# Performance work log

Hardware: AMD Instinct MI355X
Metric: run time of the kernel (lower is better)

## Reference

```python
import jax, jax.numpy as jnp
import numpy as np

EPS = 0.1
MAX_ITER = 10
N, IN_SIZE, IN_DIM = 16, 1024, 1024
HEADS, OUT_SIZE, OUT_DIM = 4, 128, 1024


def xavier(key, shape):
    fan_in, fan_out = shape[-1], int(np.prod(shape[:-1]))
    lim = float(np.sqrt(6.0 / (fan_in + fan_out)))
    return jax.random.uniform(key, shape, jnp.float32, -lim, lim)


def setup_inputs() -> dict:
    key = jax.random.key(0)
    k1, k2, k3 = jax.random.split(key, 3)
    x = jax.random.normal(k1, (N, IN_SIZE, IN_DIM), jnp.float32)
    ot_weight = xavier(k2, (HEADS, OUT_SIZE, IN_DIM))
    lin_w = xavier(k3, (OUT_DIM, HEADS * IN_DIM))
    lin_b = jnp.zeros((OUT_DIM,), jnp.float32)
    return {"x": x, "ot_weight": ot_weight, "lin_w": lin_w, "lin_b": lin_b}


def log_sinkhorn(K, max_iter):
    # K: [B, in_size, out_size] (already divided by eps)
    B, in_size, out_size = K.shape
    a = jnp.log(jnp.asarray(out_size / in_size, K.dtype))
    u = jnp.zeros((B, in_size), K.dtype)
    v = jnp.zeros((B, out_size), K.dtype)

    def body(carry, _):
        u, v = carry
        u = a - jax.nn.logsumexp(K + u[:, :, None] + v[:, None, :], axis=-1)
        v = -jax.nn.logsumexp(K + u[:, :, None] + v[:, None, :], axis=-2)
        return (u, v), None

    (u, v), _ = jax.lax.scan(body, (u, v), None, length=max_iter)
    return jnp.exp(K + u[:, :, None] + v[:, None, :])  # transport plan T


def reference(x, ot_weight, lin_w, lin_b):
    n, in_size, in_dim = x.shape
    m, out_size, _ = ot_weight.shape
    # similarity / eps : [n, m, in_size, out_size]
    K = jnp.einsum('nid,msd->nmis', x, ot_weight) / EPS
    T = log_sinkhorn(K.reshape(n * m, in_size, out_size), MAX_ITER)
    T = T.reshape(n, m, in_size, out_size)
    # weighted aggregation: [n, out_size, m, in_dim] -> [n, out_size, m*in_dim]
    feat = jnp.einsum('nmis,nid->nsmd', T, x).reshape(n, out_size, m * in_dim)
    # Linear + ReLU (Dropout is identity in eval mode)
    out = jax.nn.relu(feat @ lin_w.T + lin_b)
    return out
```

## Files before the change

### kernel.cpp

```cpp
#include <hip/hip_runtime.h>
#include <math.h>

#define EPSV 0.1f
#define MAX_ITER 10
constexpr int NB       = 16;
constexpr int IN_SIZE  = 1024;
constexpr int IN_DIM   = 1024;
constexpr int HEADS    = 4;
constexpr int OUT_SIZE = 128;
constexpr int OUT_DIM  = 1024;

typedef __attribute__((ext_vector_type(8))) _Float16 f16x8;
typedef __attribute__((ext_vector_type(4))) float f32x4;

__device__ __forceinline__ unsigned cvth2(float lo, float hi) {
    _Float16 a = (_Float16)lo, b = (_Float16)hi;
    unsigned short ua = *(unsigned short*)&a, ub = *(unsigned short*)&b;
    return (unsigned)ua | ((unsigned)ub << 16);
}
__device__ __forceinline__ unsigned short cvth1(float f) {
    _Float16 a = (_Float16)f;
    return *(unsigned short*)&a;
}
__device__ __forceinline__ unsigned short bf16rne(float f) {
    unsigned a = __float_as_uint(f);
    return (unsigned short)((a + 0x7fffu + ((a >> 16) & 1u)) >> 16);
}

template<int AMODE, bool B_F32, int CMODE, int NF, bool AKBLK, bool SWAP>
__global__ __launch_bounds__(256)
void mfma_gemm(const void* __restrict__ Ap, const void* __restrict__ Bp,
               const float* __restrict__ bias, void* __restrict__ Cp,
               int K, int lda, int ldb, int ldc, int div,
               long AsN, long AsM, long BsN, long BsM, long CsN, long CsM,
               long AkStride, float alpha)
{
    constexpr int BN  = NF * 32;
    constexpr int BKP = 40;
    const int z  = SWAP ? blockIdx.x : blockIdx.z;
    const int n0 = (SWAP ? blockIdx.z : blockIdx.x) * BN;
    const long aoff = (long)(z / div) * AsN + (long)(z % div) * AsM;
    const long boff = (long)(z / div) * BsN + (long)(z % div) * BsM;
    const long coff = (long)(z / div) * CsN + (long)(z % div) * CsM;

    __shared__ short As[128 * BKP];
    __shared__ short Bs[BN * BKP];

    const int t = threadIdx.x;
    const int lane = t & 63;
    const int w = t >> 6, wr = w >> 1, wc = w & 1;

    f32x4 acc[4][NF];
    #pragma unroll
    for (int i = 0; i < 4; ++i)
        #pragma unroll
        for (int j = 0; j < NF; ++j) { acc[i][j].x = 0.f; acc[i][j].y = 0.f; acc[i][j].z = 0.f; acc[i][j].w = 0.f; }

    for (int k0 = 0; k0 < K; k0 += 32) {
        const long abase = AKBLK ? aoff + (long)(k0 >> 10) * AkStride + (k0 & 1023)
                                 : aoff + k0;
        const long bbase = boff + k0;
        #pragma unroll
        for (int itr = 0; itr < 2; ++itr) {
            const int idx = itr * 256 + t;
            const int row = idx >> 2, kq = idx & 3;
            const uint4 p = *(const uint4*)((const short*)Ap + abase + (long)row * lda + kq * 8);
            *(uint4*)&As[row * BKP + kq * 8] = p;
        }
        #pragma unroll
        for (int itr = 0; itr < BN / 64; ++itr) {
            const int idx = itr * 256 + t;
            const int row = idx >> 2, kq = idx & 3;
            uint4 p;
            if (B_F32) {
                const float* s = (const float*)Bp + bbase + (long)(n0 + row) * ldb + kq * 8;
                const float4 f0 = *(const float4*)s, f1 = *(const float4*)(s + 4);
                p.x = cvth2(f0.x, f0.y); p.y = cvth2(f0.z, f0.w);
                p.z = cvth2(f1.x, f1.y); p.w = cvth2(f1.z, f1.w);
            } else {
                p = *(const uint4*)((const short*)Bp + bbase + (long)(n0 + row) * ldb + kq * 8);
            }
            *(uint4*)&Bs[row * BKP + kq * 8] = p;
        }
        __syncthreads();

        f16x8 af[4], bfr[NF];
        #pragma unroll
        for (int mi = 0; mi < 4; ++mi)
            af[mi] = *(const f16x8*)&As[(wr * 64 + mi * 16 + (lane & 15)) * BKP + (lane >> 4) * 8];
        #pragma unroll
        for (int ni = 0; ni < NF; ++ni)
            bfr[ni] = *(const f16x8*)&Bs[(wc * (BN / 2) + ni * 16 + (lane & 15)) * BKP + (lane >> 4) * 8];
        #pragma unroll
        for (int mi = 0; mi < 4; ++mi)
            #pragma unroll
            for (int ni = 0; ni < NF; ++ni)
                acc[mi][ni] = __builtin_amdgcn_mfma_f32_16x16x32_f16(af[mi], bfr[ni], acc[mi][ni], 0, 0, 0);
        __syncthreads();
    }

    #pragma unroll
    for (int mi = 0; mi < 4; ++mi) {
        #pragma unroll
        for (int ni = 0; ni < NF; ++ni) {
            #pragma unroll
            for (int j = 0; j < 4; ++j) {
                const int row = wr * 64 + mi * 16 + (lane >> 4) * 4 + j;
                const int col = n0 + wc * (BN / 2) + ni * 16 + (lane & 15);
                float v = acc[mi][ni][j] * alpha;
                if (CMODE == 2) { v += bias[col]; v = fmaxf(v, 0.f); }
                if (CMODE == 2 || CMODE == 4) ((float*)Cp)[coff + (long)row * ldc + col] = v;
                else ((unsigned short*)Cp)[coff + (long)row * ldc + col] = cvth1(v);
            }
        }
    }
}

__global__ __launch_bounds__(256)
void splitk_reduce(const float* __restrict__ part, const float* __restrict__ bias,
                   float* __restrict__ out)
{
    const long idx = ((long)blockIdx.x * 256 + threadIdx.x) * 4;
    const int o = (int)(idx & 1023);
    const float4 p0 = *(const float4*)(part + idx);
    const float4 p1 = *(const float4*)(part + 2097152 + idx);
    const float4 p2 = *(const float4*)(part + 2 * 2097152 + idx);
    const float4 p3 = *(const float4*)(part + 3 * 2097152 + idx);
    const float4 bv = *(const float4*)(bias + o);
    float4 r;
    r.x = fmaxf(p0.x + p1.x + p2.x + p3.x + bv.x, 0.f);
    r.y = fmaxf(p0.y + p1.y + p2.y + p3.y + bv.y, 0.f);
    r.z = fmaxf(p0.z + p1.z + p2.z + p3.z + bv.z, 0.f);
    r.w = fmaxf(p0.w + p1.w + p2.w + p3.w + bv.w, 0.f);
    *(float4*)(out + idx) = r;
}

__global__ __launch_bounds__(256)
void cvt_otw(const float* __restrict__ in, unsigned short* __restrict__ out)
{
    const long i8 = ((long)blockIdx.x * 256 + threadIdx.x) * 8;
    const float4 f0 = *(const float4*)(in + i8), f1 = *(const float4*)(in + i8 + 4);
    uint4 p;
    p.x = cvth2(f0.x, f0.y); p.y = cvth2(f0.z, f0.w);
    p.z = cvth2(f1.x, f1.y); p.w = cvth2(f1.z, f1.w);
    *(uint4*)(out + i8) = p;
}

__global__ __launch_bounds__(256)
void gemm1_exp(const unsigned short* __restrict__ otwH, const float* __restrict__ x,
               unsigned short* __restrict__ ekb, float* __restrict__ MiB)
{
    constexpr int BKP = 40;
    const int zb = blockIdx.x;
    const int nn = zb >> 2, mm = zb & 3;
    const unsigned short* A = otwH + (long)mm * (OUT_SIZE * IN_DIM);
    const float* B = x + (long)nn * (IN_SIZE * IN_DIM);
    const int n0 = blockIdx.z * 128;

    __shared__ short As[128 * BKP];
    __shared__ short Bs[128 * BKP];
    __shared__ float colmax[2][128];

    const int t = threadIdx.x;
    const int lane = t & 63;
    const int w = t >> 6, wr = w >> 1, wc = w & 1;

    f32x4 acc[4][4];
    #pragma unroll
    for (int i = 0; i < 4; ++i)
        #pragma unroll
        for (int j = 0; j < 4; ++j) { acc[i][j].x = 0.f; acc[i][j].y = 0.f; acc[i][j].z = 0.f; acc[i][j].w = 0.f; }

    for (int k0 = 0; k0 < 1024; k0 += 32) {
        #pragma unroll
        for (int itr = 0; itr < 2; ++itr) {
            const int idx = itr * 256 + t;
            const int row = idx >> 2, kq = idx & 3;
            const uint4 p = *(const uint4*)(A + (long)row * 1024 + k0 + kq * 8);
            *(uint4*)&As[row * BKP + kq * 8] = p;
        }
        #pragma unroll
        for (int itr = 0; itr < 2; ++itr) {
            const int idx = itr * 256 + t;
            const int row = idx >> 2, kq = idx & 3;
            const float* s = B + (long)(n0 + row) * 1024 + k0 + kq * 8;
            const float4 f0 = *(const float4*)s, f1 = *(const float4*)(s + 4);
            uint4 p;
            p.x = cvth2(f0.x, f0.y); p.y = cvth2(f0.z, f0.w);
            p.z = cvth2(f1.x, f1.y); p.w = cvth2(f1.z, f1.w);
            *(uint4*)&Bs[row * BKP + kq * 8] = p;
        }
        __syncthreads();

        f16x8 af[4], bfr[4];
        #pragma unroll
        for (int mi = 0; mi < 4; ++mi)
            af[mi] = *(const f16x8*)&As[(wr * 64 + mi * 16 + (lane & 15)) * BKP + (lane >> 4) * 8];
        #pragma unroll
        for (int ni = 0; ni < 4; ++ni)
            bfr[ni] = *(const f16x8*)&Bs[(wc * 64 + ni * 16 + (lane & 15)) * BKP + (lane >> 4) * 8];
        #pragma unroll
        for (int mi = 0; mi < 4; ++mi)
            #pragma unroll
            for (int ni = 0; ni < 4; ++ni)
                acc[mi][ni] = __builtin_amdgcn_mfma_f32_16x16x32_f16(af[mi], bfr[ni], acc[mi][ni], 0, 0, 0);
        __syncthreads();
    }

    float lm[4];
    #pragma unroll
    for (int ni = 0; ni < 4; ++ni) {
        float mx = -INFINITY;
        #pragma unroll
        for (int mi = 0; mi < 4; ++mi)
            #pragma unroll
            for (int j = 0; j < 4; ++j) mx = fmaxf(mx, acc[mi][ni][j]);
        mx *= 10.0f;
        mx = fmaxf(mx, __shfl_xor(mx, 16, 64));
        mx = fmaxf(mx, __shfl_xor(mx, 32, 64));
        lm[ni] = mx;
    }
    if ((lane >> 4) == 0) {
        #pragma unroll
        for (int ni = 0; ni < 4; ++ni) colmax[wr][wc * 64 + ni * 16 + lane] = lm[ni];
    }
    __syncthreads();
    float cm[4];
    #pragma unroll
    for (int ni = 0; ni < 4; ++ni) {
        const int c = wc * 64 + ni * 16 + (lane & 15);
        cm[ni] = fmaxf(colmax[0][c], colmax[1][c]);
    }
    if (wr == 0 && (lane >> 4) == 0) {
        #pragma unroll
        for (int ni = 0; ni < 4; ++ni)
            MiB[(long)zb * 1024 + n0 + wc * 64 + ni * 16 + lane] = cm[ni];
    }
    unsigned short* ekz = ekb + (long)zb * (OUT_SIZE * IN_SIZE);
    #pragma unroll
    for (int mi = 0; mi < 4; ++mi) {
        #pragma unroll
        for (int ni = 0; ni < 4; ++ni) {
            const int col = n0 + wc * 64 + ni * 16 + (lane & 15);
            #pragma unroll
            for (int j = 0; j < 4; ++j) {
                const int row = wr * 64 + mi * 16 + (lane >> 4) * 4 + j;
                ekz[(long)row * 1024 + col] = bf16rne(__expf(fmaf(acc[mi][ni][j], 10.f, -cm[ni])));
            }
        }
    }
}

__global__ __launch_bounds__(256)
void transpose_cvt(const float* __restrict__ x, unsigned short* __restrict__ xT)
{
    const int n = blockIdx.z, i0 = blockIdx.y * 64, d0 = blockIdx.x * 64;
    const float* xs = x + (long)n * (IN_SIZE * IN_DIM);
    unsigned short* xo = xT + (long)n * (IN_SIZE * IN_DIM);
    __shared__ float tile[64][65];
    const int t = threadIdx.x;
    const int r = t >> 4, c4 = (t & 15) * 4;
    #pragma unroll
    for (int rr = 0; rr < 4; ++rr) {
        const float4 v = *(const float4*)(xs + (long)(i0 + rr * 16 + r) * IN_DIM + d0 + c4);
        *(float4*)&tile[rr * 16 + r][c4] = v;
    }
    __syncthreads();
    #pragma unroll
    for (int rr = 0; rr < 4; ++rr) {
        const int dl = rr * 16 + r;
        ushort4 o;
        o.x = cvth1(tile[c4 + 0][dl]); o.y = cvth1(tile[c4 + 1][dl]);
        o.z = cvth1(tile[c4 + 2][dl]); o.w = cvth1(tile[c4 + 3][dl]);
        *(ushort4*)(xo + (long)(d0 + dl) * IN_SIZE + i0 + c4) = o;
    }
}

__global__ __launch_bounds__(1024)
void sinkhorn_split(unsigned short* __restrict__ ekb,
                    const float* __restrict__ MiB,
                    float* __restrict__ xchg, unsigned int* __restrict__ ctr)
{
    const int b = blockIdx.x;
    const int q = blockIdx.z;
    const int t = threadIdx.x;
    const int lane = t & 63, w = t >> 6;

    __shared__ unsigned ekw[128 * 129];
    __shared__ float part_u[8][256];
    __shared__ float part_v[8][128];
    __shared__ float eu_l[256];
    __shared__ float v_s[128], ev_s[128];
    __shared__ float red8[8];
    __shared__ float wg_s;

    {
        const unsigned short* src = ekb + (long)b * 131072 + q * 256;
        #pragma unroll
        for (int j = 0; j < 4; ++j) {
            const int idx = t + 1024 * j;
            const int s = idx >> 5, c8 = (idx & 31) * 8;
            const uint4 p = *(const uint4*)(src + (long)s * 1024 + c8);
            const int bd = s * 129 + (c8 >> 1);
            ekw[bd] = p.x; ekw[bd + 1] = p.y; ekw[bd + 2] = p.z; ekw[bd + 3] = p.w;
        }
    }
    float mi_t = 0.f, u_reg = 0.f, w_t = 0.f;
    if (t < 256) mi_t = MiB[(long)b * 1024 + q * 256 + t];
    if (t < 128) { v_s[t] = 0.f; ev_s[t] = 1.0f; }
    __syncthreads();

    const float A0 = -2.0794415416798357f;
    float vmx = 0.f;

    for (int it = 0; it < MAX_ITER; ++it) {
        {
            const int p = t & 127, sq = t >> 7;
            float s0 = 0.f, s1 = 0.f;
            #pragma unroll
            for (int j = 0; j < 16; ++j) {
                const int s = sq * 16 + j;
                const unsigned e = ekw[s * 129 + p];
                const float evv = ev_s[s];
                s0 = fmaf(__uint_as_float(e << 16),          evv, s0);
                s1 = fmaf(__uint_as_float(e & 0xffff0000u),  evv, s1);
            }
            part_u[sq][2 * p]     = s0;
            part_u[sq][2 * p + 1] = s1;
        }
        __syncthreads();

        if (t < 256) {
            float S = part_u[0][t];
            #pragma unroll
            for (int g = 1; g < 8; ++g) S += part_u[g][t];
            const float un = A0 - u_reg - mi_t - vmx - __logf(S);
            u_reg = un;
            w_t = mi_t + un;
            float wl = w_t;
            #pragma unroll
            for (int m = 1; m < 64; m <<= 1) wl = fmaxf(wl, __shfl_xor(wl, m, 64));
            if (lane == 0) red8[4 + w] = wl;
        }
        __syncthreads();
        const float wmx_l = fmaxf(fmaxf(red8[4], red8[5]), fmaxf(red8[6], red8[7]));
        if (t < 256) eu_l[t] = __expf(w_t - wmx_l);
        __syncthreads();

        {
            const int s = t & 127, g = t >> 7;
            float acc = 0.f;
            #pragma unroll
            for (int j = 0; j < 16; ++j) {
                const int p = 16 * g + j;
                const unsigned e = ekw[s * 129 + p];
                const float2 eup = *(const float2*)&eu_l[2 * p];
                acc = fmaf(__uint_as_float(e << 16),         eup.x, acc);
                acc = fmaf(__uint_as_float(e & 0xffff0000u), eup.y, acc);
            }
            part_v[g][s] = acc;
        }
        __syncthreads();

        float* slot = xchg + ((long)(b * MAX_ITER + it) * 4 + q) * 160;
        if (t < 128) {
            float cp_l = part_v[0][t];
            #pragma unroll
            for (int g = 1; g < 8; ++g) cp_l += part_v[g][t];
            __hip_atomic_store(slot + t, cp_l, __ATOMIC_RELAXED, __HIP_MEMORY_SCOPE_AGENT);
        }
        if (t == 0)
            __hip_atomic_store(slot + 128, wmx_l, __ATOMIC_RELAXED, __HIP_MEMORY_SCOPE_AGENT);
        __syncthreads();
        if (t == 0) {
            unsigned int* c = ctr + b * MAX_ITER + it;
            __hip_atomic_fetch_add(c, 1u, __ATOMIC_RELEASE, __HIP_MEMORY_SCOPE_AGENT);
            while (__hip_atomic_load(c, __ATOMIC_RELAXED, __HIP_MEMORY_SCOPE_AGENT) < 4u) {}
            (void)__hip_atomic_load(c, __ATOMIC_ACQUIRE, __HIP_MEMORY_SCOPE_AGENT);
        }
        __syncthreads();

        if (t < 128) {
            float* base = xchg + (long)(b * MAX_ITER + it) * 4 * 160;
            const float w0 = __hip_atomic_load(base + 0 * 160 + 128, __ATOMIC_RELAXED, __HIP_MEMORY_SCOPE_AGENT);
            const float w1 = __hip_atomic_load(base + 1 * 160 + 128, __ATOMIC_RELAXED, __HIP_MEMORY_SCOPE_AGENT);
            const float w2 = __hip_atomic_load(base + 2 * 160 + 128, __ATOMIC_RELAXED, __HIP_MEMORY_SCOPE_AGENT);
            const float w3 = __hip_atomic_load(base + 3 * 160 + 128, __ATOMIC_RELAXED, __HIP_MEMORY_SCOPE_AGENT);
            const float wg = fmaxf(fmaxf(w0, w1), fmaxf(w2, w3));
            const float c0 = __hip_atomic_load(base + 0 * 160 + t, __ATOMIC_RELAXED, __HIP_MEMORY_SCOPE_AGENT);
            const float c1 = __hip_atomic_load(base + 1 * 160 + t, __ATOMIC_RELAXED, __HIP_MEMORY_SCOPE_AGENT);
            const float c2 = __hip_atomic_load(base + 2 * 160 + t, __ATOMIC_RELAXED, __HIP_MEMORY_SCOPE_AGENT);
            const float c3 = __hip_atomic_load(base + 3 * 160 + t, __ATOMIC_RELAXED, __HIP_MEMORY_SCOPE_AGENT);
            const float cp = c0 * __expf(w0 - wg) + c1 * __expf(w1 - wg)
                           + c2 * __expf(w2 - wg) + c3 * __expf(w3 - wg);
            const float vn = -v_s[t] - wg - __logf(cp);
            v_s[t] = vn;
            if (t == 0) wg_s = wg;
            float xv = vn;
            #pragma unroll
            for (int m = 1; m < 64; m <<= 1) xv = fmaxf(xv, __shfl_xor(xv, m, 64));
            if (lane == 0) red8[w] = xv;
        }
        __syncthreads();
        vmx = fmaxf(red8[0], red8[1]);
        if (t < 128) ev_s[t] = __expf(v_s[t] - vmx);
        __syncthreads();
    }

    const float wg = wg_s;
    if (t < 256) eu_l[t] = __expf(w_t - wg);
    if (t < 128) ev_s[t] = __expf(v_s[t] + wg);
    __syncthreads();
    unsigned short* To = ekb + (long)b * 131072 + q * 256;
    #pragma unroll
    for (int j = 0; j < 16; ++j) {
        const int idx = t + 1024 * j;
        const int s  = idx >> 7;
        const int ip = idx & 127;
        const unsigned e = ekw[s * 129 + ip];
        const float2 eup = *(const float2*)&eu_l[2 * ip];
        const float ec = ev_s[s];
        const float lo = __uint_as_float(e << 16)         * eup.x * ec;
        const float hi = __uint_as_float(e & 0xffff0000u) * eup.y * ec;
        *(unsigned*)(To + (long)s * 1024 + ip * 2) = cvth2(lo, hi);
    }
}

extern "C" void kernel_launch(void* const* d_in, const int* in_sizes, int n_in,
                              void* d_out, int out_size, void* d_ws, size_t ws_size,
                              hipStream_t stream)
{
    const float* x     = (const float*)d_in[0];
    const float* otw   = (const float*)d_in[1];
    const float* lin_w = (const float*)d_in[2];
    const float* lin_b = (const float*)d_in[3];
    float* out = (float*)d_out;

    unsigned short* xT   = (unsigned short*)d_ws;
    unsigned short* ekb  = xT + 16777216;
    unsigned short* feat = ekb + 8388608;
    float* partial = (float*)d_ws;
    float* MiB  = (float*)d_out;
    float* xchg = MiB + 131072;
    unsigned int* ctrB = (unsigned int*)(MiB + 655360);
    unsigned short* otwH = (unsigned short*)(MiB + 786432);

    hipMemsetAsync(ctrB, 0, 64 * MAX_ITER * sizeof(unsigned int), stream);

    cvt_otw<<<dim3(256), 256, 0, stream>>>(otw, otwH);

    transpose_cvt<<<dim3(16, 16, NB), 256, 0, stream>>>(x, xT);

    gemm1_exp<<<dim3(64, 1, 8), 256, 0, stream>>>(otwH, x, ekb, MiB);

    sinkhorn_split<<<dim3(64, 1, 4), 1024, 0, stream>>>(ekb, MiB, xchg, ctrB);

    mfma_gemm<0, false, 1, 4, false, true><<<dim3(64, 1, 8), 256, 0, stream>>>(
        ekb, xT, nullptr, feat,
        1024, 1024, 1024, 1024, 4,
        524288, 131072, 1048576, 0, 524288, 131072, 0, 1.0f);

    mfma_gemm<0, true, 4, 2, false, false><<<dim3(16, 1, 64), 256, 0, stream>>>(
        feat, lin_w, nullptr, partial,
        1024, 1024, 4096, 1024, 16,
        131072, 524288, 1024, 0, 2097152, 131072, 0, 1.0f);

    splitk_reduce<<<dim3(2048), 256, 0, stream>>>(partial, lin_b, out);
}
```

Before: 210.3 us.

## Use direct global-to-LDS loads and pre-convert x to fp16 for gemm1

Replaces the register-staged global→LDS tile copies in the fp16 GEMM paths with global_load_lds 16-byte direct loads, dropping the padded LDS stride to 32. Adds a separate kernel that converts x to fp16 before gemm1_exp, so that gemm1 can also use direct LDS loads instead of loading fp32 and converting in the loop. xH shares workspace with xT, so gemm1 is moved ahead of transpose_cvt. The unpadded stride may add LDS bank conflicts on fragment reads, and the extra conversion pass writes and rereads x.

```diff
diff --git a/kernel.cpp b/kernel.cpp
--- a/kernel.cpp
+++ b/kernel.cpp
@@ -26,8 +26,13 @@
     unsigned a = __float_as_uint(f);
     return (unsigned short)((a + 0x7fffu + ((a >> 16) & 1u)) >> 16);
 }
-
-template<int AMODE, bool B_F32, int CMODE, int NF, bool AKBLK, bool SWAP>
+__device__ __forceinline__ void glds16(const void* g, void* l) {
+    __builtin_amdgcn_global_load_lds(
+        (const __attribute__((address_space(1))) unsigned int*)g,
+        (__attribute__((address_space(3))) unsigned int*)l, 16, 0, 0);
+}
+
+template<bool B_F32, int CMODE, int NF, bool AKBLK, bool SWAP>
 __global__ __launch_bounds__(256)
 void mfma_gemm(const void* __restrict__ Ap, const void* __restrict__ Bp,
                const float* __restrict__ bias, void* __restrict__ Cp,
@@ -35,16 +40,16 @@
                long AsN, long AsM, long BsN, long BsM, long CsN, long CsM,
                long AkStride, float alpha)
 {
-    constexpr int BN  = NF * 32;
-    constexpr int BKP = 40;
+    constexpr int BN   = NF * 32;
+    constexpr int BSTR = B_F32 ? 40 : 32;
     const int z  = SWAP ? blockIdx.x : blockIdx.z;
     const int n0 = (SWAP ? blockIdx.z : blockIdx.x) * BN;
     const long aoff = (long)(z / div) * AsN + (long)(z % div) * AsM;
     const long boff = (long)(z / div) * BsN + (long)(z % div) * BsM;
     const long coff = (long)(z / div) * CsN + (long)(z % div) * CsM;
 
-    __shared__ short As[128 * BKP];
-    __shared__ short Bs[BN * BKP];
+    __shared__ short As[128 * 32];
+    __shared__ short Bs[BN * BSTR];
 
     const int t = threadIdx.x;
     const int lane = t & 63;
@@ -55,42 +60,48 @@
     for (int i = 0; i < 4; ++i)
         #pragma unroll
         for (int j = 0; j < NF; ++j) { acc[i][j].x = 0.f; acc[i][j].y = 0.f; acc[i][j].z = 0.f; acc[i][j].w = 0.f; }
+
+    const int lrow = lane >> 2, lce = (lane & 3) * 8;
 
     for (int k0 = 0; k0 < K; k0 += 32) {
         const long abase = AKBLK ? aoff + (long)(k0 >> 10) * AkStride + (k0 & 1023)
                                  : aoff + k0;
         const long bbase = boff + k0;
         #pragma unroll
-        for (int itr = 0; itr < 2; ++itr) {
-            const int idx = itr * 256 + t;
-            const int row = idx >> 2, kq = idx & 3;
-            const uint4 p = *(const uint4*)((const short*)Ap + abase + (long)row * lda + kq * 8);
-            *(uint4*)&As[row * BKP + kq * 8] = p;
-        }
-        #pragma unroll
-        for (int itr = 0; itr < BN / 64; ++itr) {
-            const int idx = itr * 256 + t;
-            const int row = idx >> 2, kq = idx & 3;
-            uint4 p;
-            if (B_F32) {
+        for (int j = 0; j < 2; ++j) {
+            const int row0 = (w * 2 + j) * 16;
+            glds16((const short*)Ap + abase + (long)(row0 + lrow) * lda + lce,
+                   &As[row0 * 32]);
+        }
+        if (B_F32) {
+            #pragma unroll
+            for (int itr = 0; itr < BN / 64; ++itr) {
+                const int idx = itr * 256 + t;
+                const int row = idx >> 2, kq = idx & 3;
                 const float* s = (const float*)Bp + bbase + (long)(n0 + row) * ldb + kq * 8;
                 const float4 f0 = *(const float4*)s, f1 = *(const float4*)(s + 4);
+                uint4 p;
                 p.x = cvth2(f0.x, f0.y); p.y = cvth2(f0.z, f0.w);
                 p.z = cvth2(f1.x, f1.y); p.w = cvth2(f1.z, f1.w);
-            } else {
-                p = *(const uint4*)((const short*)Bp + bbase + (long)(n0 + row) * ldb + kq * 8);
-            }
-            *(uint4*)&Bs[row * BKP + kq * 8] = p;
+                *(uint4*)&Bs[row * BSTR + kq * 8] = p;
+            }
+        } else {
+            #pragma unroll
+            for (int j = 0; j < BN / 64; ++j) {
+                const int row0 = (w * (BN / 64) + j) * 16;
+                glds16((const short*)Bp + bbase + (long)(n0 + row0 + lrow) * ldb + lce,
+                       &Bs[row0 * 32]);
+            }
         }
         __syncthreads();
 
         f16x8 af[4], bfr[NF];
         #pragma unroll
         for (int mi = 0; mi < 4; ++mi)
-            af[mi] = *(const f16x8*)&As[(wr * 64 + mi * 16 + (lane & 15)) * BKP + (lane >> 4) * 8];
+            af[mi] = *(const f16x8*)&As[(wr * 64 + mi * 16 + (lane & 15)) * 32 + (lane >> 4) * 8];
         #pragma unroll
         for (int ni = 0; ni < NF; ++ni)
-            bfr[ni] = *(const f16x8*)&Bs[(wc * (BN / 2) + ni * 16 + (lane & 15)) * BKP + (lane >> 4) * 8];
+            bfr[ni] = *(const f16x8*)&Bs[(wc * (BN / 2) + ni * 16 + (lane & 15)) * BSTR + (lane >> 4) * 8];
         #pragma unroll
         for (int mi = 0; mi < 4; ++mi)
             #pragma unroll
@@ -136,7 +147,7 @@
 }
 
 __global__ __launch_bounds__(256)
-void cvt_otw(const float* __restrict__ in, unsigned short* __restrict__ out)
+void cvt_f16(const float* __restrict__ in, unsigned short* __restrict__ out)
 {
     const long i8 = ((long)blockIdx.x * 256 + threadIdx.x) * 8;
     const float4 f0 = *(const float4*)(in + i8), f1 = *(const float4*)(in + i8 + 4);
@@ -147,23 +158,24 @@
 }
 
 __global__ __launch_bounds__(256)
-void gemm1_exp(const unsigned short* __restrict__ otwH, const float* __restrict__ x,
+void gemm1_exp(const unsigned short* __restrict__ otwH,
+               const unsigned short* __restrict__ xH,
                unsigned short* __restrict__ ekb, float* __restrict__ MiB)
 {
-    constexpr int BKP = 40;
     const int zb = blockIdx.x;
     const int nn = zb >> 2, mm = zb & 3;
     const unsigned short* A = otwH + (long)mm * (OUT_SIZE * IN_DIM);
-    const float* B = x + (long)nn * (IN_SIZE * IN_DIM);
+    const unsigned short* B = xH + (long)nn * (IN_SIZE * IN_DIM);
     const int n0 = blockIdx.z * 128;
 
-    __shared__ short As[128 * BKP];
-    __shared__ short Bs[128 * BKP];
+    __shared__ short As[128 * 32];
+    __shared__ short Bs[128 * 32];
     __shared__ float colmax[2][128];
 
     const int t = threadIdx.x;
     const int lane = t & 63;
     const int w = t >> 6, wr = w >> 1, wc = w & 1;
+    const int lrow = lane >> 2, lce = (lane & 3) * 8;
 
     f32x4 acc[4][4];
     #pragma unroll
@@ -173,32 +185,24 @@
 
     for (int k0 = 0; k0 < 1024; k0 += 32) {
         #pragma unroll
-        for (int itr = 0; itr < 2; ++itr) {
-            const int idx = itr * 256 + t;
-            const int row = idx >> 2, kq = idx & 3;
-            const uint4 p = *(const uint4*)(A + (long)row * 1024 + k0 + kq * 8);
-            *(uint4*)&As[row * BKP + kq * 8] = p;
-        }
-        #pragma unroll
-        for (int itr = 0; itr < 2; ++itr) {
-            const int idx = itr * 256 + t;
-            const int row = idx >> 2, kq = idx & 3;
-            const float* s = B + (long)(n0 + row) * 1024 + k0 + kq * 8;
-            const float4 f0 = *(const float4*)s, f1 = *(const float4*)(s + 4);
-            uint4 p;
-            p.x = cvth2(f0.x, f0.y); p.y = cvth2(f0.z, f0.w);
-            p.z = cvth2(f1.x, f1.y); p.w = cvth2(f1.z, f1.w);
-            *(uint4*)&Bs[row * BKP + kq * 8] = p;
+        for (int j = 0; j < 2; ++j) {
+            const int row0 = (w * 2 + j) * 16;
+            glds16(A + (long)(row0 + lrow) * 1024 + k0 + lce, &As[row0 * 32]);
+        }
+        #pragma unroll
+        for (int j = 0; j < 2; ++j) {
+            const int row0 = (w * 2 + j) * 16;
+            glds16(B + (long)(n0 + row0 + lrow) * 1024 + k0 + lce, &Bs[row0 * 32]);
         }
         __syncthreads();
 
         f16x8 af[4], bfr[4];
         #pragma unroll
         for (int mi = 0; mi < 4; ++mi)
-            af[mi] = *(const f16x8*)&As[(wr * 64 + mi * 16 + (lane & 15)) * BKP + (lane >> 4) * 8];
+            af[mi] = *(const f16x8*)&As[(wr * 64 + mi * 16 + (lane & 15)) * 32 + (lane >> 4) * 8];
         #pragma unroll
         for (int ni = 0; ni < 4; ++ni)
-            bfr[ni] = *(const f16x8*)&Bs[(wc * 64 + ni * 16 + (lane & 15)) * BKP + (lane >> 4) * 8];
+            bfr[ni] = *(const f16x8*)&Bs[(wc * 64 + ni * 16 + (lane & 15)) * 32 + (lane >> 4) * 8];
         #pragma unroll
         for (int mi = 0; mi < 4; ++mi)
             #pragma unroll
@@ -436,8 +440,9 @@
     const float* lin_b = (const float*)d_in[3];
     float* out = (float*)d_out;
 
+    unsigned short* xH   = (unsigned short*)d_ws;
     unsigned short* xT   = (unsigned short*)d_ws;
-    unsigned short* ekb  = xT + 16777216;
+    unsigned short* ekb  = xH + 16777216;
     unsigned short* feat = ekb + 8388608;
     float* partial = (float*)d_ws;
     float* MiB  = (float*)d_out;
@@ -447,20 +452,21 @@
 
     hipMemsetAsync(ctrB, 0, 64 * MAX_ITER * sizeof(unsigned int), stream);
 
-    cvt_otw<<<dim3(256), 256, 0, stream>>>(otw, otwH);
+    cvt_f16<<<dim3(256), 256, 0, stream>>>(otw, otwH);
+    cvt_f16<<<dim3(8192), 256, 0, stream>>>(x, xH);
+
+    gemm1_exp<<<dim3(64, 1, 8), 256, 0, stream>>>(otwH, xH, ekb, MiB);
 
     transpose_cvt<<<dim3(16, 16, NB), 256, 0, stream>>>(x, xT);
 
-    gemm1_exp<<<dim3(64, 1, 8), 256, 0, stream>>>(otwH, x, ekb, MiB);
-
     sinkhorn_split<<<dim3(64, 1, 4), 1024, 0, stream>>>(ekb, MiB, xchg, ctrB);
 
-    mfma_gemm<0, false, 1, 4, false, true><<<dim3(64, 1, 8), 256, 0, stream>>>(
+    mfma_gemm<false, 1, 4, false, true><<<dim3(64, 1, 8), 256, 0, stream>>>(
         ekb, xT, nullptr, feat,
         1024, 1024, 1024, 1024, 4,
         524288, 131072, 1048576, 0, 524288, 131072, 0, 1.0f);
 
-    mfma_gemm<0, true, 4, 2, false, false><<<dim3(16, 1, 64), 256, 0, stream>>>(
+    mfma_gemm<true, 4, 2, false, false><<<dim3(16, 1, 64), 256, 0, stream>>>(
         feat, lin_w, nullptr, partial,
         1024, 1024, 4096, 1024, 16,
         131072, 524288, 1024, 0, 2097152, 131072, 0, 1.0f);
```

New measurement: 208.2 us. No clear change (-1.0%).
